# Optimization experiments

Hardware: AMD Instinct MI355X
Metric: run time of the kernel (lower is better)

The kernel has to match this reference:

```python
import jax, jax.numpy as jnp
import numpy as np

N_HEAD = 16
W = 128  # one-sided window = attention_window // 2


def setup_inputs() -> dict:
    key = jax.random.key(0)
    ks = jax.random.split(key, 6)
    B, S, D = 4, 1536, 1024
    init = lambda k: jax.random.normal(k, (D, D), jnp.float32) * 0.02
    return {
        "x": jax.random.normal(ks[0], (B, S, D), jnp.float32),
        "Wq": init(ks[1]), "bq": jnp.zeros((D,), jnp.float32),
        "Wk": init(ks[2]),
        "Wv": init(ks[3]), "bv": jnp.zeros((D,), jnp.float32),
        "Wo": init(ks[4]), "bo": jnp.zeros((D,), jnp.float32),
    }


def _local_attention(q, k, v, w):
    """Sliding-window attention. q,k,v: [B,H,S,Dh]; q,k pre-scaled.
    Returns context [B,H,S,Dh] and banded logits qk [B,S,H,2w+1] (fp32)."""
    B, H, S, Dh = q.shape
    C = S // w  # number of w-sized query chunks
    pad = [(0, 0), (0, 0), (w, w), (0, 0)]
    kp = jnp.pad(k, pad)
    vp = jnp.pad(v, pad)
    # key/value chunks: chunk c sees padded positions [c*w, c*w + 3w)
    idx = jnp.arange(C)[:, None] * w + jnp.arange(3 * w)[None, :]  # [C,3w]
    kc = kp[:, :, idx]                      # [B,H,C,3w,Dh]
    vc = vp[:, :, idx]                      # [B,H,C,3w,Dh]
    qc = q.reshape(B, H, C, w, Dh)          # [B,H,C,w,Dh]
    scores = jnp.einsum('bhcxd,bhcyd->bhcxy', qc, kc)  # [B,H,C,w,3w]
    # extract diagonal band: query x attends to chunk-local keys y = x .. x+2w
    xi = jnp.arange(w)[:, None]             # [w,1]
    jj = jnp.arange(2 * w + 1)[None, :]     # [1,2w+1]
    y = xi + jj                             # [w,2w+1], values in [0,3w)
    band = jnp.take_along_axis(scores, y[None, None, None], axis=-1)  # [B,H,C,w,2w+1]
    # mask positions whose absolute key index falls outside [0,S)
    key_pos = jnp.arange(C)[:, None, None] * w + xi[None] + jj[None] - w  # [C,w,2w+1]
    valid = (key_pos >= 0) & (key_pos < S)
    band = jnp.where(valid[None, None], band, -jnp.inf)
    prob = jax.nn.softmax(band.astype(jnp.float32), axis=-1).astype(q.dtype)
    # scatter band probs back to chunk layout, then contract with value chunks
    scat = jnp.zeros_like(scores).at[..., xi, y].set(prob)  # [B,H,C,w,3w]
    ctx = jnp.einsum('bhcxy,bhcyd->bhcxd', scat, vc).reshape(B, H, S, Dh)
    qk = band.astype(jnp.float32).reshape(B, H, S, 2 * w + 1).transpose(0, 2, 1, 3)
    return ctx, qk


def reference(x, Wq, bq, Wk, Wv, bv, Wo, bo):
    B, S, D = x.shape
    H, Dh = N_HEAD, D // N_HEAD
    scale = Dh ** (-0.25)
    q = ((x @ Wq.T + bq).reshape(B, S, H, Dh).transpose(0, 2, 1, 3)) * scale
    k = ((x @ Wk.T).reshape(B, S, H, Dh).transpose(0, 2, 1, 3)) * scale
    v = (x @ Wv.T + bv).reshape(B, S, H, Dh).transpose(0, 2, 1, 3)
    ctx, qk = _local_attention(q, k, v, W)
    wv = ctx.transpose(0, 2, 1, 3).reshape(B, S, D)
    out = wv @ Wo.T + bo
    return out, qk
```

## Files before the change

### kernel.cpp

```cpp
#include <hip/hip_runtime.h>

#define S_LEN  1536
#define NH     16
#define DHEAD  64
#define WIN    128
#define BAND   257
#define DMODEL 1024
#define BATCH  4
#define MROWS  (BATCH * S_LEN)

#define SQ    32
#define SWIN  (SQ + 2*WIN)
#define WKEYS 320
#define DCHUNK 32

#define NEG_BIG (-3.0e38f)

typedef __attribute__((ext_vector_type(8))) short frag_ab;
typedef __attribute__((ext_vector_type(4))) float frag_cd;
typedef __attribute__((ext_vector_type(8))) unsigned short ushort8v;

__device__ __forceinline__ unsigned short f2bf(float f) {
  unsigned u = __float_as_uint(f);
  u += 0x7FFFu + ((u >> 16) & 1u);
  return (unsigned short)(u >> 16);
}
__device__ __forceinline__ float bf2f(unsigned short h) {
  return __uint_as_float(((unsigned)h) << 16);
}

__device__ __forceinline__ void gload16(const unsigned short* g, unsigned short* l) {
  __builtin_amdgcn_global_load_lds(
      (const __attribute__((address_space(1))) unsigned int*)g,
      (__attribute__((address_space(3))) unsigned int*)l, 16, 0, 0);
}

__global__ __launch_bounds__(256)
void convert_hilo(const float* __restrict__ src, unsigned short* __restrict__ hi,
                  unsigned short* __restrict__ lo, int n4)
{
  const int i = blockIdx.x * 256 + threadIdx.x;
  if (i >= n4) return;
  const float4 v = reinterpret_cast<const float4*>(src)[i];
  unsigned short h0 = f2bf(v.x), h1 = f2bf(v.y), h2 = f2bf(v.z), h3 = f2bf(v.w);
  unsigned short l0 = f2bf(v.x - bf2f(h0)), l1 = f2bf(v.y - bf2f(h1));
  unsigned short l2 = f2bf(v.z - bf2f(h2)), l3 = f2bf(v.w - bf2f(h3));
  uint2 hp, lp;
  hp.x = (unsigned)h0 | ((unsigned)h1 << 16); hp.y = (unsigned)h2 | ((unsigned)h3 << 16);
  lp.x = (unsigned)l0 | ((unsigned)l1 << 16); lp.y = (unsigned)l2 | ((unsigned)l3 << 16);
  reinterpret_cast<uint2*>(hi)[i] = hp;
  reinterpret_cast<uint2*>(lo)[i] = lp;
}

__global__ __launch_bounds__(256)
void mfma_gemm_bt(const unsigned short* __restrict__ Ah_g,
                  const unsigned short* __restrict__ Al_g,
                  const unsigned short* __restrict__ Bh_g,
                  const unsigned short* __restrict__ Bl_g,
                  const float* __restrict__ bias, float scale,
                  float* __restrict__ Cf,
                  unsigned short* __restrict__ Ch,
                  unsigned short* __restrict__ Cl, int mode)
{
  __shared__ __align__(16) unsigned short Ah[128*32];
  __shared__ __align__(16) unsigned short Al[128*32];
  __shared__ __align__(16) unsigned short Bh[64*32];
  __shared__ __align__(16) unsigned short Bl[64*32];

  const int t    = threadIdx.x;
  const int wave = t >> 6, lane = t & 63;
  const int wr   = wave >> 1, wc = wave & 1;
  const int m0   = blockIdx.y * 128;
  const int n0   = blockIdx.x * 64;

  frag_cd acc[4][2];
#pragma unroll
  for (int i = 0; i < 4; ++i)
#pragma unroll
    for (int j = 0; j < 2; ++j) acc[i][j] = (frag_cd){0.f,0.f,0.f,0.f};

  const int srow = lane >> 2;
  const int scol = (lane & 3) * 8;
  const unsigned short* pa0 = Ah_g + (size_t)(m0 + wave*32      + srow) * DMODEL + scol;
  const unsigned short* pa1 = Ah_g + (size_t)(m0 + wave*32 + 16 + srow) * DMODEL + scol;
  const unsigned short* qa0 = Al_g + (size_t)(m0 + wave*32      + srow) * DMODEL + scol;
  const unsigned short* qa1 = Al_g + (size_t)(m0 + wave*32 + 16 + srow) * DMODEL + scol;
  const unsigned short* pb  = Bh_g + (size_t)(n0 + wave*16      + srow) * DMODEL + scol;
  const unsigned short* qb  = Bl_g + (size_t)(n0 + wave*16      + srow) * DMODEL + scol;
  unsigned short* lA0 = &Ah[(wave*32)*32];
  unsigned short* lA1 = &Ah[(wave*32+16)*32];
  unsigned short* lL0 = &Al[(wave*32)*32];
  unsigned short* lL1 = &Al[(wave*32+16)*32];
  unsigned short* lB  = &Bh[(wave*16)*32];
  unsigned short* lBl = &Bl[(wave*16)*32];

  const int l16  = lane & 15;
  const int koff = (lane >> 4) * 8;
  int ofsA[4], ofsB[2];
#pragma unroll
  for (int i = 0; i < 4; ++i) ofsA[i] = (wr*64 + i*16 + l16)*32 + koff;
#pragma unroll
  for (int j = 0; j < 2; ++j) ofsB[j] = (wc*32 + j*16 + l16)*32 + koff;

  for (int k0 = 0; k0 < DMODEL; k0 += 32) {
    gload16(pa0, lA0); gload16(pa1, lA1);
    gload16(qa0, lL0); gload16(qa1, lL1);
    gload16(pb,  lB);  gload16(qb,  lBl);
    pa0 += 32; pa1 += 32; qa0 += 32; qa1 += 32; pb += 32; qb += 32;
    __syncthreads();

    frag_ab ah[4], alr[4], bh[2], blr[2];
#pragma unroll
    for (int i = 0; i < 4; ++i) {
      ah[i]  = *reinterpret_cast<const frag_ab*>(&Ah[ofsA[i]]);
      alr[i] = *reinterpret_cast<const frag_ab*>(&Al[ofsA[i]]);
    }
#pragma unroll
    for (int j = 0; j < 2; ++j) {
      bh[j]  = *reinterpret_cast<const frag_ab*>(&Bh[ofsB[j]]);
      blr[j] = *reinterpret_cast<const frag_ab*>(&Bl[ofsB[j]]);
    }
#pragma unroll
    for (int i = 0; i < 4; ++i)
#pragma unroll
      for (int j = 0; j < 2; ++j) {
        acc[i][j] = __builtin_amdgcn_mfma_f32_16x16x32_bf16(ah[i],  bh[j],  acc[i][j], 0,0,0);
        acc[i][j] = __builtin_amdgcn_mfma_f32_16x16x32_bf16(ah[i],  blr[j], acc[i][j], 0,0,0);
        acc[i][j] = __builtin_amdgcn_mfma_f32_16x16x32_bf16(alr[i], bh[j],  acc[i][j], 0,0,0);
      }
    __syncthreads();
  }

  const int rg = lane >> 4;
#pragma unroll
  for (int j = 0; j < 2; ++j) {
    const int n = n0 + wc*32 + j*16 + l16;
    const float bval = bias ? bias[n] : 0.f;
#pragma unroll
    for (int i = 0; i < 4; ++i) {
#pragma unroll
      for (int r = 0; r < 4; ++r) {
        const int m = m0 + wr*64 + i*16 + rg*4 + r;
        const float v = (acc[i][j][r] + bval) * scale;
        if (mode) {
          const int b = m / S_LEN;
          const int s = m - b * S_LEN;
          const int hh = n >> 6, dh = n & 63;
          const size_t idx = ((size_t)((b*NH + hh)*S_LEN + s))*DHEAD + dh;
          const unsigned short hv = f2bf(v);
          Ch[idx] = hv;
          Cl[idx] = f2bf(v - bf2f(hv));
        } else {
          Cf[(size_t)m * DMODEL + n] = v;
        }
      }
    }
  }
}

__global__ __launch_bounds__(256)
void mfma_scores(const unsigned short* __restrict__ Qh_g,
                 const unsigned short* __restrict__ Ql_g,
                 const unsigned short* __restrict__ Kh_g,
                 const unsigned short* __restrict__ Kl_g,
                 float* __restrict__ qk)
{
  __shared__ __align__(16) unsigned short Qhs[SQ*32],    Qls[SQ*32];
  __shared__ __align__(16) unsigned short Khs[WKEYS*32], Kls[WKEYS*32];

  const int t    = threadIdx.x;
  const int wave = t >> 6, lane = t & 63;
  const int qa0  = blockIdx.x * SQ;
  const int h    = blockIdx.y, b = blockIdx.z;
  const int ws0  = qa0 - WIN;
  const size_t ho = (size_t)(b*NH + h) * S_LEN * DHEAD;
  const unsigned short* Qh = Qh_g + ho;
  const unsigned short* Ql = Ql_g + ho;
  const unsigned short* Kh = Kh_g + ho;
  const unsigned short* Kl = Kl_g + ho;

  const int l16  = lane & 15;
  const int koff = (lane >> 4) * 8;
  const int srow = lane >> 2;
  const int scol = (lane & 3) * 8;

  frag_cd acc[2][5];
#pragma unroll
  for (int tm = 0; tm < 2; ++tm)
#pragma unroll
    for (int tn = 0; tn < 5; ++tn) acc[tm][tn] = (frag_cd){0.f,0.f,0.f,0.f};

  for (int p = 0; p < 2; ++p) {
    const int d0 = p * 32;
    if (p) __syncthreads();
#pragma unroll
    for (int i = 0; i < 5; ++i) {
      const int r0 = wave*80 + i*16;
      const ptrdiff_t g = (ptrdiff_t)(ws0 + r0 + srow) * DHEAD + d0 + scol;
      gload16(Kh + g, &Khs[r0*32]);
      gload16(Kl + g, &Kls[r0*32]);
    }
    if (wave < 2) {
      const unsigned short* src = wave ? Ql : Qh;
      unsigned short* dst = wave ? Qls : Qhs;
#pragma unroll
      for (int i = 0; i < 2; ++i) {
        const ptrdiff_t g = (ptrdiff_t)(qa0 + i*16 + srow) * DHEAD + d0 + scol;
        gload16(src + g, &dst[i*16*32]);
      }
    }
    __syncthreads();

    frag_ab ah[2], al[2];
#pragma unroll
    for (int tm = 0; tm < 2; ++tm) {
      const int o = (tm*16 + l16)*32 + koff;
      ah[tm] = *reinterpret_cast<const frag_ab*>(&Qhs[o]);
      al[tm] = *reinterpret_cast<const frag_ab*>(&Qls[o]);
    }
#pragma unroll
    for (int tn = 0; tn < 5; ++tn) {
      const int o = (wave*80 + tn*16 + l16)*32 + koff;
      frag_ab bh = *reinterpret_cast<const frag_ab*>(&Khs[o]);
      frag_ab bl = *reinterpret_cast<const frag_ab*>(&Kls[o]);
#pragma unroll
      for (int tm = 0; tm < 2; ++tm) {
        acc[tm][tn] = __builtin_amdgcn_mfma_f32_16x16x32_bf16(ah[tm], bh, acc[tm][tn], 0,0,0);
        acc[tm][tn] = __builtin_amdgcn_mfma_f32_16x16x32_bf16(ah[tm], bl, acc[tm][tn], 0,0,0);
        acc[tm][tn] = __builtin_amdgcn_mfma_f32_16x16x32_bf16(al[tm], bh, acc[tm][tn], 0,0,0);
      }
    }
  }

  const int rg = (lane >> 4) * 4;
#pragma unroll
  for (int tm = 0; tm < 2; ++tm) {
#pragma unroll
    for (int r = 0; r < 4; ++r) {
      const int x = tm*16 + rg + r;
      float* qrow = qk + ((size_t)(b*S_LEN + qa0 + x)*NH + h) * BAND;
#pragma unroll
      for (int tn = 0; tn < 5; ++tn) {
        const int yw = wave*80 + tn*16 + l16;
        const int j = yw - x;
        if (j >= 0 && j < BAND) {
          const int kp = ws0 + yw;
          qrow[j] = (kp >= 0 && kp < S_LEN) ? acc[tm][tn][r] : NEG_BIG;
        }
      }
    }
  }
}

__global__ __launch_bounds__(256)
void ctx_kernel(const unsigned short* __restrict__ Vh_g,
                const unsigned short* __restrict__ Vl_g,
                const float* __restrict__ qk,
                unsigned short* __restrict__ ctx_hi, unsigned short* __restrict__ ctx_lo)
{
  __shared__ __align__(16) unsigned short Pth[SQ][SWIN];
  __shared__ __align__(16) unsigned short Ptl[SQ][SWIN];
  __shared__ __align__(16) unsigned short Vth[DCHUNK][SWIN];
  __shared__ __align__(16) unsigned short Vtl[DCHUNK][SWIN];

  const int t    = threadIdx.x;
  const int wave = t >> 6, lane = t & 63;
  const int qa0  = blockIdx.x * SQ;
  const int h    = blockIdx.y, b = blockIdx.z;
  const int ws0  = qa0 - WIN;
  const size_t ho = (size_t)(b*NH + h) * S_LEN * DHEAD;
  const unsigned short* Vh = Vh_g + ho;
  const unsigned short* Vl = Vl_g + ho;

  {
    const uint4 z = make_uint4(0u,0u,0u,0u);
    uint4* p0 = reinterpret_cast<uint4*>(&Pth[0][0]);
    uint4* p1 = reinterpret_cast<uint4*>(&Ptl[0][0]);
    for (int i = t; i < (SQ*SWIN)/8; i += 256) { p0[i] = z; p1[i] = z; }
  }
  __syncthreads();

  for (int qq = 0; qq < 8; ++qq) {
    const int x = wave*8 + qq;
    const float* qrow = qk + ((size_t)(b*S_LEN + qa0 + x)*NH + h) * BAND;
    float vals[5];
    float mx = NEG_BIG;
#pragma unroll
    for (int it = 0; it < 5; ++it) {
      const int j = lane + it*64;
      vals[it] = (j < BAND) ? qrow[j] : NEG_BIG;
      mx = fmaxf(mx, vals[it]);
    }
#pragma unroll
    for (int off = 32; off > 0; off >>= 1) mx = fmaxf(mx, __shfl_xor(mx, off, 64));
    float ss = 0.f;
#pragma unroll
    for (int it = 0; it < 5; ++it) {
      const int j = lane + it*64;
      const float e = (j < BAND) ? __expf(vals[it] - mx) : 0.f;
      vals[it] = e; ss += e;
    }
#pragma unroll
    for (int off = 32; off > 0; off >>= 1) ss += __shfl_xor(ss, off, 64);
    const float inv = 1.f / ss;
#pragma unroll
    for (int it = 0; it < 5; ++it) {
      const int j = lane + it*64;
      if (j < BAND) {
        const float p = vals[it] * inv;
        const unsigned short ph = f2bf(p);
        Pth[x][x + j] = ph;
        Ptl[x][x + j] = f2bf(p - bf2f(ph));
      }
    }
  }

  const int l16  = lane & 15;
  const int koff = (lane >> 4) * 8;
  const int wr   = wave >> 1;
  const int wc   = wave & 1;

  for (int chunk = 0; chunk < 2; ++chunk) {
    const int d0 = chunk * DCHUNK;
    __syncthreads();

#pragma unroll
    for (int half = 0; half < 2; ++half) {
      const unsigned short* src = half ? Vl : Vh;
      unsigned short (*dst)[SWIN] = half ? Vtl : Vth;
      for (int yb = 0; yb < SWIN; yb += 64) {
        const int y = yb + lane;
        if (y < SWIN) {
          const int kp = ws0 + y;
          ushort8v v = {0,0,0,0,0,0,0,0};
          if (kp >= 0 && kp < S_LEN)
            v = *reinterpret_cast<const ushort8v*>(src + (size_t)kp*DHEAD + d0 + wave*8);
#pragma unroll
          for (int e = 0; e < 8; ++e) dst[wave*8 + e][y] = v[e];
        }
      }
    }
    __syncthreads();

    frag_cd acc = (frag_cd){0.f,0.f,0.f,0.f};
#pragma unroll
    for (int ks = 0; ks < SWIN/32; ++ks) {
      const int kk = ks*32 + koff;
      frag_ab ah = *reinterpret_cast<const frag_ab*>(&Pth[wr*16 + l16][kk]);
      frag_ab al = *reinterpret_cast<const frag_ab*>(&Ptl[wr*16 + l16][kk]);
      frag_ab bh = *reinterpret_cast<const frag_ab*>(&Vth[wc*16 + l16][kk]);
      frag_ab bl = *reinterpret_cast<const frag_ab*>(&Vtl[wc*16 + l16][kk]);
      acc = __builtin_amdgcn_mfma_f32_16x16x32_bf16(ah, bh, acc, 0,0,0);
      acc = __builtin_amdgcn_mfma_f32_16x16x32_bf16(ah, bl, acc, 0,0,0);
      acc = __builtin_amdgcn_mfma_f32_16x16x32_bf16(al, bh, acc, 0,0,0);
    }

    const int d  = d0 + wc*16 + l16;
    const int rg = (lane >> 4) * 4;
#pragma unroll
    for (int r = 0; r < 4; ++r) {
      const int x = wr*16 + rg + r;
      const size_t idx = ((size_t)(b*S_LEN + qa0 + x))*DMODEL + h*DHEAD + d;
      const float v = acc[r];
      const unsigned short hv = f2bf(v);
      ctx_hi[idx] = hv;
      ctx_lo[idx] = f2bf(v - bf2f(hv));
    }
  }
}

extern "C" void kernel_launch(void* const* d_in, const int* in_sizes, int n_in,
                              void* d_out, int out_size, void* d_ws, size_t ws_size,
                              hipStream_t stream) {
  const float* x  = (const float*)d_in[0];
  const float* Wq = (const float*)d_in[1];
  const float* bq = (const float*)d_in[2];
  const float* Wk = (const float*)d_in[3];
  const float* Wv = (const float*)d_in[4];
  const float* bv = (const float*)d_in[5];
  const float* Wo = (const float*)d_in[6];
  const float* bo = (const float*)d_in[7];

  float* out = (float*)d_out;
  float* qk  = out + (size_t)MROWS * DMODEL;

  const size_t NX = (size_t)MROWS * DMODEL;
  const size_t NW = (size_t)DMODEL * DMODEL;

  unsigned short* xh  = (unsigned short*)qk;
  unsigned short* xl  = xh  + NX;
  unsigned short* wqh = xl  + NX;
  unsigned short* wql = wqh + NW;
  unsigned short* wkh = wql + NW;
  unsigned short* wkl = wkh + NW;
  unsigned short* wvh = wkl + NW;
  unsigned short* wvl = wvh + NW;

  unsigned short* Qh = (unsigned short*)d_ws;
  unsigned short* Ql = Qh + NX;
  unsigned short* Kh = Ql + NX;
  unsigned short* Kl = Kh + NX;
  unsigned short* Vh = Kl + NX;
  unsigned short* Vl = Vh + NX;
  unsigned short* ctxh = Qh;
  unsigned short* ctxl = Ql;
  unsigned short* woh  = Kh;
  unsigned short* wol  = Kh + NW;

  const float scale = 0.35355339059327373f;

  dim3 blk(256);
  hipLaunchKernelGGL(convert_hilo, dim3(NX/1024), blk, 0, stream, x,  xh,  xl,  (int)(NX/4));
  hipLaunchKernelGGL(convert_hilo, dim3(NW/1024), blk, 0, stream, Wq, wqh, wql, (int)(NW/4));
  hipLaunchKernelGGL(convert_hilo, dim3(NW/1024), blk, 0, stream, Wk, wkh, wkl, (int)(NW/4));
  hipLaunchKernelGGL(convert_hilo, dim3(NW/1024), blk, 0, stream, Wv, wvh, wvl, (int)(NW/4));

  dim3 gg(DMODEL/64, MROWS/128);
  hipLaunchKernelGGL(mfma_gemm_bt, gg, blk, 0, stream, xh, xl, wqh, wql, bq,      scale,
                     (float*)nullptr, Qh, Ql, 1);
  hipLaunchKernelGGL(mfma_gemm_bt, gg, blk, 0, stream, xh, xl, wkh, wkl, nullptr, scale,
                     (float*)nullptr, Kh, Kl, 1);
  hipLaunchKernelGGL(mfma_gemm_bt, gg, blk, 0, stream, xh, xl, wvh, wvl, bv,      1.0f,
                     (float*)nullptr, Vh, Vl, 1);

  dim3 ga(S_LEN/SQ, NH, BATCH);
  hipLaunchKernelGGL(mfma_scores, ga, blk, 0, stream, Qh, Ql, Kh, Kl, qk);

  hipLaunchKernelGGL(convert_hilo, dim3(NW/1024), blk, 0, stream, Wo, woh, wol, (int)(NW/4));
  hipLaunchKernelGGL(ctx_kernel, ga, blk, 0, stream, Vh, Vl, qk, ctxh, ctxl);

  hipLaunchKernelGGL(mfma_gemm_bt, gg, blk, 0, stream, ctxh, ctxl, woh, wol, bo, 1.0f,
                     out, (unsigned short*)nullptr, (unsigned short*)nullptr, 0);
}
```

Measured before the change: 553.3 us.

## Fuse banded score computation, softmax and context GEMM into one attention kernel

Merges the score kernel and the context kernel into one block that keeps the logits in registers and computes the softmax through cross-wave shared-memory reductions. This avoids re-reading the fp32 banded logits from global memory, and V tiles are double-buffered through registers while the previous chunk's MFMAs run. It also remaps block indices so each XCD handles a contiguous range of query blocks, likely for L2 locality. Because ctx now lives in the output buffer, the final GEMM writes to workspace and needs an extra full copy kernel, and only half the waves do MFMA in the context stage.

```diff
diff --git a/kernel.cpp b/kernel.cpp
--- a/kernel.cpp
+++ b/kernel.cpp
@@ -12,7 +12,7 @@
 #define SQ    32
 #define SWIN  (SQ + 2*WIN)
 #define WKEYS 320
-#define DCHUNK 32
+#define PST   296
 
 #define NEG_BIG (-3.0e38f)
 
@@ -53,6 +53,13 @@
 }
 
 __global__ __launch_bounds__(256)
+void copy_f4(const float4* __restrict__ src, float4* __restrict__ dst, int n4)
+{
+  const int i = blockIdx.x * 256 + threadIdx.x;
+  if (i < n4) dst[i] = src[i];
+}
+
+__global__ __launch_bounds__(256)
 void mfma_gemm_bt(const unsigned short* __restrict__ Ah_g,
                   const unsigned short* __restrict__ Al_g,
                   const unsigned short* __restrict__ Bh_g,
@@ -159,28 +166,46 @@
 }
 
 __global__ __launch_bounds__(256)
-void mfma_scores(const unsigned short* __restrict__ Qh_g,
-                 const unsigned short* __restrict__ Ql_g,
-                 const unsigned short* __restrict__ Kh_g,
-                 const unsigned short* __restrict__ Kl_g,
-                 float* __restrict__ qk)
+void attn_fused(const unsigned short* __restrict__ Qh_g, const unsigned short* __restrict__ Ql_g,
+                const unsigned short* __restrict__ Kh_g, const unsigned short* __restrict__ Kl_g,
+                const unsigned short* __restrict__ Vh_g, const unsigned short* __restrict__ Vl_g,
+                float* __restrict__ qk,
+                unsigned short* __restrict__ ctx_hi, unsigned short* __restrict__ ctx_lo)
 {
-  __shared__ __align__(16) unsigned short Qhs[SQ*32],    Qls[SQ*32];
-  __shared__ __align__(16) unsigned short Khs[WKEYS*32], Kls[WKEYS*32];
+  __shared__ __align__(16) unsigned char arena[59904];
+  unsigned short* Khs = (unsigned short*)(arena);
+  unsigned short* Kls = (unsigned short*)(arena + 20480);
+  unsigned short* Qhs = (unsigned short*)(arena + 40960);
+  unsigned short* Qls = (unsigned short*)(arena + 43008);
+  unsigned short* Pth = (unsigned short*)(arena);
+  unsigned short* Ptl = (unsigned short*)(arena + 18944);
+  float*          red = (float*)(arena + 37888);
+  unsigned short* Vth = (unsigned short*)(arena + 40960);
+  unsigned short* Vtl = (unsigned short*)(arena + 50432);
 
   const int t    = threadIdx.x;
   const int wave = t >> 6, lane = t & 63;
-  const int qa0  = blockIdx.x * SQ;
-  const int h    = blockIdx.y, b = blockIdx.z;
+
+  const int lid  = blockIdx.x;
+  const int xcd  = lid & 7;
+  const int idx  = lid >> 3;
+  const int qblk = xcd*6 + (idx % 6);
+  const int hb   = idx / 6;
+  const int h    = hb & 15, b = hb >> 4;
+  const int qa0  = qblk * SQ;
   const int ws0  = qa0 - WIN;
+
   const size_t ho = (size_t)(b*NH + h) * S_LEN * DHEAD;
   const unsigned short* Qh = Qh_g + ho;
   const unsigned short* Ql = Ql_g + ho;
   const unsigned short* Kh = Kh_g + ho;
   const unsigned short* Kl = Kl_g + ho;
+  const unsigned short* Vh = Vh_g + ho;
+  const unsigned short* Vl = Vl_g + ho;
 
   const int l16  = lane & 15;
-  const int koff = (lane >> 4) * 8;
+  const int grp  = lane >> 4;
+  const int koff = grp * 8;
   const int srow = lane >> 2;
   const int scol = (lane & 3) * 8;
 
@@ -232,139 +257,168 @@
     }
   }
 
-  const int rg = (lane >> 4) * 4;
-#pragma unroll
-  for (int tm = 0; tm < 2; ++tm) {
+#pragma unroll
+  for (int tm = 0; tm < 2; ++tm)
+#pragma unroll
+    for (int tn = 0; tn < 5; ++tn)
+#pragma unroll
+      for (int r = 0; r < 4; ++r) {
+        const int x  = tm*16 + grp*4 + r;
+        const int yw = wave*80 + tn*16 + l16;
+        const int j  = yw - x;
+        const int kp = ws0 + yw;
+        const bool ok = (j >= 0) & (j < BAND) & (kp >= 0) & (kp < S_LEN);
+        acc[tm][tn][r] = ok ? acc[tm][tn][r] : NEG_BIG;
+      }
+#pragma unroll
+  for (int tm = 0; tm < 2; ++tm)
 #pragma unroll
     for (int r = 0; r < 4; ++r) {
-      const int x = tm*16 + rg + r;
+      const int x = tm*16 + grp*4 + r;
       float* qrow = qk + ((size_t)(b*S_LEN + qa0 + x)*NH + h) * BAND;
 #pragma unroll
       for (int tn = 0; tn < 5; ++tn) {
         const int yw = wave*80 + tn*16 + l16;
-        const int j = yw - x;
-        if (j >= 0 && j < BAND) {
-          const int kp = ws0 + yw;
-          qrow[j] = (kp >= 0 && kp < S_LEN) ? acc[tm][tn][r] : NEG_BIG;
-        }
-      }
-    }
-  }
-}
-
-__global__ __launch_bounds__(256)
-void ctx_kernel(const unsigned short* __restrict__ Vh_g,
-                const unsigned short* __restrict__ Vl_g,
-                const float* __restrict__ qk,
-                unsigned short* __restrict__ ctx_hi, unsigned short* __restrict__ ctx_lo)
-{
-  __shared__ __align__(16) unsigned short Pth[SQ][SWIN];
-  __shared__ __align__(16) unsigned short Ptl[SQ][SWIN];
-  __shared__ __align__(16) unsigned short Vth[DCHUNK][SWIN];
-  __shared__ __align__(16) unsigned short Vtl[DCHUNK][SWIN];
-
-  const int t    = threadIdx.x;
-  const int wave = t >> 6, lane = t & 63;
-  const int qa0  = blockIdx.x * SQ;
-  const int h    = blockIdx.y, b = blockIdx.z;
-  const int ws0  = qa0 - WIN;
-  const size_t ho = (size_t)(b*NH + h) * S_LEN * DHEAD;
-  const unsigned short* Vh = Vh_g + ho;
-  const unsigned short* Vl = Vl_g + ho;
-
+        const int j  = yw - x;
+        if (j >= 0 && j < BAND) qrow[j] = acc[tm][tn][r];
+      }
+    }
+
+  __syncthreads();
+
+  ushort8v vreg[5];
+  const unsigned short* vsrc = (wave & 2) ? Vl : Vh;
+  unsigned short*       vdst = (wave & 2) ? Vtl : Vth;
+  const int dsub = (wave & 1) * 8;
+
+  auto loadV = [&](int c) {
+    const int d0 = c*16 + dsub;
+#pragma unroll
+    for (int it = 0; it < 5; ++it) {
+      const int y = it*64 + lane;
+      ushort8v v = {0,0,0,0,0,0,0,0};
+      if (y < SWIN) {
+        const int kp = ws0 + y;
+        if (kp >= 0 && kp < S_LEN)
+          v = *reinterpret_cast<const ushort8v*>(vsrc + (size_t)kp*DHEAD + d0);
+      }
+      vreg[it] = v;
+    }
+  };
+  auto writeV = [&]() {
+#pragma unroll
+    for (int it = 0; it < 5; ++it) {
+      const int y = it*64 + lane;
+      if (y < SWIN) {
+#pragma unroll
+        for (int e = 0; e < 8; ++e) vdst[(dsub+e)*PST + y] = vreg[it][e];
+      }
+    }
+  };
+
+  loadV(0);
+  float gm[2][4];
+#pragma unroll
+  for (int tm = 0; tm < 2; ++tm)
+#pragma unroll
+    for (int r = 0; r < 4; ++r) {
+      float m = acc[tm][0][r];
+#pragma unroll
+      for (int tn = 1; tn < 5; ++tn) m = fmaxf(m, acc[tm][tn][r]);
+      m = fmaxf(m, __shfl_xor(m, 1, 64));
+      m = fmaxf(m, __shfl_xor(m, 2, 64));
+      m = fmaxf(m, __shfl_xor(m, 4, 64));
+      m = fmaxf(m, __shfl_xor(m, 8, 64));
+      gm[tm][r] = m;
+      if (l16 == 0) red[(0*4 + wave)*32 + tm*16 + grp*4 + r] = m;
+    }
   {
     const uint4 z = make_uint4(0u,0u,0u,0u);
-    uint4* p0 = reinterpret_cast<uint4*>(&Pth[0][0]);
-    uint4* p1 = reinterpret_cast<uint4*>(&Ptl[0][0]);
-    for (int i = t; i < (SQ*SWIN)/8; i += 256) { p0[i] = z; p1[i] = z; }
+    uint4* pz = reinterpret_cast<uint4*>(arena);
+    for (int i = t; i < 37888/16; i += 256) pz[i] = z;
   }
+  writeV();
+  loadV(1);
   __syncthreads();
 
-  for (int qq = 0; qq < 8; ++qq) {
-    const int x = wave*8 + qq;
-    const float* qrow = qk + ((size_t)(b*S_LEN + qa0 + x)*NH + h) * BAND;
-    float vals[5];
-    float mx = NEG_BIG;
-#pragma unroll
-    for (int it = 0; it < 5; ++it) {
-      const int j = lane + it*64;
-      vals[it] = (j < BAND) ? qrow[j] : NEG_BIG;
-      mx = fmaxf(mx, vals[it]);
-    }
-#pragma unroll
-    for (int off = 32; off > 0; off >>= 1) mx = fmaxf(mx, __shfl_xor(mx, off, 64));
-    float ss = 0.f;
-#pragma unroll
-    for (int it = 0; it < 5; ++it) {
-      const int j = lane + it*64;
-      const float e = (j < BAND) ? __expf(vals[it] - mx) : 0.f;
-      vals[it] = e; ss += e;
-    }
-#pragma unroll
-    for (int off = 32; off > 0; off >>= 1) ss += __shfl_xor(ss, off, 64);
-    const float inv = 1.f / ss;
-#pragma unroll
-    for (int it = 0; it < 5; ++it) {
-      const int j = lane + it*64;
-      if (j < BAND) {
-        const float p = vals[it] * inv;
-        const unsigned short ph = f2bf(p);
-        Pth[x][x + j] = ph;
-        Ptl[x][x + j] = f2bf(p - bf2f(ph));
-      }
-    }
-  }
-
-  const int l16  = lane & 15;
-  const int koff = (lane >> 4) * 8;
-  const int wr   = wave >> 1;
-  const int wc   = wave & 1;
-
-  for (int chunk = 0; chunk < 2; ++chunk) {
-    const int d0 = chunk * DCHUNK;
+#pragma unroll
+  for (int tm = 0; tm < 2; ++tm)
+#pragma unroll
+    for (int r = 0; r < 4; ++r) {
+      const int x = tm*16 + grp*4 + r;
+      float m = red[0*128 + 0*32 + x];
+      m = fmaxf(m, red[0*128 + 1*32 + x]);
+      m = fmaxf(m, red[0*128 + 2*32 + x]);
+      m = fmaxf(m, red[0*128 + 3*32 + x]);
+      gm[tm][r] = m;
+      float s = 0.f;
+#pragma unroll
+      for (int tn = 0; tn < 5; ++tn) {
+        const float e = __expf(acc[tm][tn][r] - m);
+        acc[tm][tn][r] = e;
+        s += e;
+      }
+      s += __shfl_xor(s, 1, 64);
+      s += __shfl_xor(s, 2, 64);
+      s += __shfl_xor(s, 4, 64);
+      s += __shfl_xor(s, 8, 64);
+      if (l16 == 0) red[(1*4 + wave)*32 + x] = s;
+    }
+  __syncthreads();
+
+#pragma unroll
+  for (int tm = 0; tm < 2; ++tm)
+#pragma unroll
+    for (int r = 0; r < 4; ++r) {
+      const int x = tm*16 + grp*4 + r;
+      const float gs = red[128 + 0*32 + x] + red[128 + 1*32 + x]
+                     + red[128 + 2*32 + x] + red[128 + 3*32 + x];
+      const float inv = 1.f / gs;
+#pragma unroll
+      for (int tn = 0; tn < 5; ++tn) {
+        const int yw = wave*80 + tn*16 + l16;
+        const int j  = yw - x;
+        if (yw < SWIN && j >= 0 && j < BAND) {
+          const float p = acc[tm][tn][r] * inv;
+          const unsigned short ph = f2bf(p);
+          Pth[x*PST + yw] = ph;
+          Ptl[x*PST + yw] = f2bf(p - bf2f(ph));
+        }
+      }
+    }
+  __syncthreads();
+
+  for (int c = 0; c < 4; ++c) {
+    if ((wave & 1) == 0) {
+      const int wr = wave >> 1;
+      frag_cd a = (frag_cd){0.f,0.f,0.f,0.f};
+#pragma unroll
+      for (int ks = 0; ks < SWIN/32; ++ks) {
+        const int kk = ks*32 + koff;
+        frag_ab ph = *reinterpret_cast<const frag_ab*>(&Pth[(wr*16 + l16)*PST + kk]);
+        frag_ab pl = *reinterpret_cast<const frag_ab*>(&Ptl[(wr*16 + l16)*PST + kk]);
+        frag_ab vh = *reinterpret_cast<const frag_ab*>(&Vth[l16*PST + kk]);
+        frag_ab vl = *reinterpret_cast<const frag_ab*>(&Vtl[l16*PST + kk]);
+        a = __builtin_amdgcn_mfma_f32_16x16x32_bf16(ph, vh, a, 0,0,0);
+        a = __builtin_amdgcn_mfma_f32_16x16x32_bf16(ph, vl, a, 0,0,0);
+        a = __builtin_amdgcn_mfma_f32_16x16x32_bf16(pl, vh, a, 0,0,0);
+      }
+      const int d = c*16 + l16;
+#pragma unroll
+      for (int r = 0; r < 4; ++r) {
+        const int x = wr*16 + grp*4 + r;
+        const size_t oidx = ((size_t)(b*S_LEN + qa0 + x))*DMODEL + h*DHEAD + d;
+        const float v = a[r];
+        const unsigned short hv = f2bf(v);
+        ctx_hi[oidx] = hv;
+        ctx_lo[oidx] = f2bf(v - bf2f(hv));
+      }
+    }
     __syncthreads();
-
-#pragma unroll
-    for (int half = 0; half < 2; ++half) {
-      const unsigned short* src = half ? Vl : Vh;
-      unsigned short (*dst)[SWIN] = half ? Vtl : Vth;
-      for (int yb = 0; yb < SWIN; yb += 64) {
-        const int y = yb + lane;
-        if (y < SWIN) {
-          const int kp = ws0 + y;
-          ushort8v v = {0,0,0,0,0,0,0,0};
-          if (kp >= 0 && kp < S_LEN)
-            v = *reinterpret_cast<const ushort8v*>(src + (size_t)kp*DHEAD + d0 + wave*8);
-#pragma unroll
-          for (int e = 0; e < 8; ++e) dst[wave*8 + e][y] = v[e];
-        }
-      }
-    }
-    __syncthreads();
-
-    frag_cd acc = (frag_cd){0.f,0.f,0.f,0.f};
-#pragma unroll
-    for (int ks = 0; ks < SWIN/32; ++ks) {
-      const int kk = ks*32 + koff;
-      frag_ab ah = *reinterpret_cast<const frag_ab*>(&Pth[wr*16 + l16][kk]);
-      frag_ab al = *reinterpret_cast<const frag_ab*>(&Ptl[wr*16 + l16][kk]);
-      frag_ab bh = *reinterpret_cast<const frag_ab*>(&Vth[wc*16 + l16][kk]);
-      frag_ab bl = *reinterpret_cast<const frag_ab*>(&Vtl[wc*16 + l16][kk]);
-      acc = __builtin_amdgcn_mfma_f32_16x16x32_bf16(ah, bh, acc, 0,0,0);
-      acc = __builtin_amdgcn_mfma_f32_16x16x32_bf16(ah, bl, acc, 0,0,0);
-      acc = __builtin_amdgcn_mfma_f32_16x16x32_bf16(al, bh, acc, 0,0,0);
-    }
-
-    const int d  = d0 + wc*16 + l16;
-    const int rg = (lane >> 4) * 4;
-#pragma unroll
-    for (int r = 0; r < 4; ++r) {
-      const int x = wr*16 + rg + r;
-      const size_t idx = ((size_t)(b*S_LEN + qa0 + x))*DMODEL + h*DHEAD + d;
-      const float v = acc[r];
-      const unsigned short hv = f2bf(v);
-      ctx_hi[idx] = hv;
-      ctx_lo[idx] = f2bf(v - bf2f(hv));
+    if (c < 3) {
+      writeV();
+      if (c < 2) loadV(c + 2);
+      __syncthreads();
     }
   }
 }
@@ -402,10 +456,12 @@
   unsigned short* Kl = Kh + NX;
   unsigned short* Vh = Kl + NX;
   unsigned short* Vl = Vh + NX;
-  unsigned short* ctxh = Qh;
-  unsigned short* ctxl = Ql;
+
+  unsigned short* ctxh = (unsigned short*)out;
+  unsigned short* ctxl = ctxh + NX;
   unsigned short* woh  = Kh;
   unsigned short* wol  = Kh + NW;
+  float* outTmp = (float*)d_ws;
 
   const float scale = 0.35355339059327373f;
 
@@ -423,12 +479,13 @@
   hipLaunchKernelGGL(mfma_gemm_bt, gg, blk, 0, stream, xh, xl, wvh, wvl, bv,      1.0f,
                      (float*)nullptr, Vh, Vl, 1);
 
-  dim3 ga(S_LEN/SQ, NH, BATCH);
-  hipLaunchKernelGGL(mfma_scores, ga, blk, 0, stream, Qh, Ql, Kh, Kl, qk);
+  hipLaunchKernelGGL(attn_fused, dim3((S_LEN/SQ)*NH*BATCH), blk, 0, stream,
+                     Qh, Ql, Kh, Kl, Vh, Vl, qk, ctxh, ctxl);
 
   hipLaunchKernelGGL(convert_hilo, dim3(NW/1024), blk, 0, stream, Wo, woh, wol, (int)(NW/4));
-  hipLaunchKernelGGL(ctx_kernel, ga, blk, 0, stream, Vh, Vl, qk, ctxh, ctxl);
 
   hipLaunchKernelGGL(mfma_gemm_bt, gg, blk, 0, stream, ctxh, ctxl, woh, wol, bo, 1.0f,
-                     out, (unsigned short*)nullptr, (unsigned short*)nullptr, 0);
-}
+                     outTmp, (unsigned short*)nullptr, (unsigned short*)nullptr, 0);
+  hipLaunchKernelGGL(copy_f4, dim3(NX/1024), blk, 0, stream,
+                     (const float4*)outTmp, (float4*)out, (int)(NX/4));
+}
```

Measured after the change: 509.7 us. 7.9% less time.
